# Optimization experiments

Measured on AMD Instinct MI355X. Metric: run time of the kernel, lower is better.

The kernel has to match this reference:

```python
import jax, jax.numpy as jnp
import numpy as np

B, T, D = 8, 16, 1024
N, K, H = 16, 8, 128   # q heads, kv heads, head dim
S = 8192               # cache size
CUR = 4096             # tokens already in cache
ROPE_THETA = 1000000
EPS = 1e-6
LARGE_NEGATIVE = jnp.finfo(jnp.bfloat16).min


def setup_inputs() -> dict:
    key = jax.random.key(0)
    ks = jax.random.split(key, 8)
    w = 0.02  # realistic weight scale
    return {
        "x": jax.random.normal(ks[0], (B, T, D), jnp.float32),
        "Wq": jax.random.normal(ks[1], (D, N, H), jnp.float32) * w,
        "Wk": jax.random.normal(ks[2], (D, K, H), jnp.float32) * w,
        "Wv": jax.random.normal(ks[3], (D, K, H), jnp.float32) * w,
        "Wo": jax.random.normal(ks[4], (N, H, D), jnp.float32) * w,
        "q_scale": jnp.ones((H,), jnp.float32),
        "k_scale": jnp.ones((H,), jnp.float32),
        "k_cache": jax.random.normal(ks[5], (B, S, K, H), jnp.float32),
        "v_cache": jax.random.normal(ks[6], (B, S, K, H), jnp.float32),
        "segment_ids": jnp.ones((B, T), jnp.int32),
        "start_ind": jnp.zeros((B,), jnp.int32),  # already resolved (= left_pads)
        "cur_ind": CUR,
    }


def _rmsnorm(x, scale, eps=EPS):
    xf = x.astype(jnp.float32)
    y = xf * jax.lax.rsqrt(jnp.mean(xf * xf, axis=-1, keepdims=True) + eps)
    return (y * scale).astype(x.dtype)


def _rope_sincos(positions, head_dim):
    frac = jnp.arange(0, head_dim, 2, dtype=jnp.float32) / head_dim
    inv_freq = 1.0 / (ROPE_THETA ** frac)
    ang = jnp.einsum("BT,k->BTk", positions.astype(jnp.float32), inv_freq,
                     precision=jax.lax.Precision.HIGHEST)
    return jnp.sin(ang), jnp.cos(ang)


def _apply_rope(x, sin, cos):
    x1, x2 = x[..., : x.shape[-1] // 2], x[..., x.shape[-1] // 2 :]
    sin, cos = sin[:, :, None, :], cos[:, :, None, :]
    return jnp.concatenate([x1 * cos - x2 * sin, x2 * cos + x1 * sin], axis=-1).astype(x.dtype)


def reference(x, Wq, Wk, Wv, Wo, q_scale, k_scale, k_cache, v_cache,
              segment_ids, start_ind, cur_ind):
    b, t, _ = x.shape
    n_rep = N // K
    scale = H ** -0.5

    # projections + per-head RMSNorm on q/k
    q = _rmsnorm(jnp.einsum("BTD,DNH->BTNH", x, Wq), q_scale)
    k = _rmsnorm(jnp.einsum("BSD,DKH->BSKH", x, Wk), k_scale)
    v = jnp.einsum("BSD,DKH->BSKH", x, Wv)

    # start index: resolved from left pads on first call
    left_pads = jnp.sum(jnp.cumsum(segment_ids != 0, axis=-1) == 0, -1).astype(jnp.int32)
    start = jnp.where(start_ind < 0, left_pads, start_ind)

    # positions from segment ids, offset by cache cursor
    rel = jax.vmap(lambda row: jnp.where(row != 0, jnp.arange(t) - jnp.argmax(row), 2 ** 30))(segment_ids)
    pos = rel + cur_ind
    sin, cos = _rope_sincos(pos, H)
    q = _apply_rope(q, sin, cos)
    k = _apply_rope(k, sin, cos)

    # KV cache append
    kc = jax.lax.dynamic_update_slice(k_cache, k, (0, cur_ind, 0, 0))
    vc = jax.lax.dynamic_update_slice(v_cache, v, (0, cur_ind, 0, 0))

    # GQA attention against full cache
    qg = q.reshape((b, t, K, n_rep, H))
    logits = jnp.einsum("BTKGH,BSKH->BTSKG", qg, kc) * scale

    q_pos = cur_ind + jnp.arange(t, dtype=jnp.int32)[None, :] - start[:, None]
    ts = jnp.arange(S, dtype=jnp.int32)
    kv_seg = (ts[None, :] >= start[:, None]) & (ts[None, :] < cur_ind + t)
    k_pos = ts[None, :] - start[:, None]
    causal = k_pos[:, None, :] <= q_pos[:, :, None]
    seg_mask = kv_seg[:, None, :] == segment_ids[:, :, None]
    mask = (causal & seg_mask)[:, :, :, None, None]

    logits = jnp.where(mask, logits, LARGE_NEGATIVE)
    w = jax.nn.softmax(logits.astype(jnp.float32), axis=2).astype(logits.dtype)
    o = jnp.einsum("BTSKG,BSKH->BTKGH", w, vc).reshape((b, t, N, H))
    return jnp.einsum("BTNH,NHD->BTD", o, Wo)
```

## Files before the change

kernel.cpp:

```cpp
#include <hip/hip_runtime.h>

#define BB 8
#define TT 16
#define DD 1024
#define NN 16
#define KHN 8
#define HH 128
#define SS 8192
#define NPART 8

typedef __attribute__((ext_vector_type(8))) short bf16x8;
typedef __attribute__((ext_vector_type(4))) float f32x4;

__device__ __forceinline__ unsigned short f2bf(float f) {
  unsigned u = __builtin_bit_cast(unsigned, f);
  u += 0x7FFFu + ((u >> 16) & 1u);
  return (unsigned short)(u >> 16);
}
__device__ __forceinline__ float bf2f(unsigned short h) {
  unsigned u = ((unsigned)h) << 16;
  return __builtin_bit_cast(float, u);
}
__device__ __forceinline__ f32x4 mfma16(bf16x8 a, bf16x8 b, f32x4 c) {
  return __builtin_amdgcn_mfma_f32_16x16x32_bf16(a, b, c, 0, 0, 0);
}
__device__ __forceinline__ void pack4(unsigned short* dst, float a, float b, float c, float d) {
  unsigned lo = (unsigned)f2bf(a) | ((unsigned)f2bf(b) << 16);
  unsigned hi = (unsigned)f2bf(c) | ((unsigned)f2bf(d) << 16);
  *(uint2*)dst = make_uint2(lo, hi);
}

__global__ __launch_bounds__(256) void k_qkv_gemm(
    const float* __restrict__ x, const float* __restrict__ Wq,
    const float* __restrict__ Wk, const float* __restrict__ Wv,
    float* __restrict__ qkv) {
  __shared__ __align__(16) unsigned short Al[32][40];
  __shared__ __align__(16) unsigned short Bl[32][132];
  const int tid = threadIdx.x;
  const int lane = tid & 63, wv = tid >> 6;
  const int cc = lane & 15, g = lane >> 4;
  const int m0 = blockIdx.x * 32;
  const int cbk = blockIdx.y;
  const float* Wsrc;
  int ldw, n0;
  if (cbk < 16)      { Wsrc = Wq; ldw = 2048; n0 = cbk * 128; }
  else if (cbk < 24) { Wsrc = Wk; ldw = 1024; n0 = (cbk - 16) * 128; }
  else               { Wsrc = Wv; ldw = 1024; n0 = (cbk - 24) * 128; }
  const int rt = wv >> 1, cb0 = (wv & 1) * 64;
  f32x4 acc[4];
#pragma unroll
  for (int i = 0; i < 4; ++i) acc[i] = (f32x4)0.0f;

  for (int k0 = 0; k0 < 1024; k0 += 32) {
    {
      int r = tid >> 3, c4 = (tid & 7) << 2;
      float4 f = *(const float4*)(x + (m0 + r) * 1024 + k0 + c4);
      pack4(&Al[r][c4], f.x, f.y, f.z, f.w);
    }
#pragma unroll
    for (int i = 0; i < 4; ++i) {
      int ch = tid + (i << 8);
      int r = ch >> 5, c4 = (ch & 31) << 2;
      float4 f = *(const float4*)(Wsrc + (size_t)(k0 + r) * ldw + n0 + c4);
      pack4(&Bl[r][c4], f.x, f.y, f.z, f.w);
    }
    __syncthreads();
    bf16x8 af = *(const bf16x8*)&Al[rt * 16 + cc][g * 8];
#pragma unroll
    for (int ct = 0; ct < 4; ++ct) {
      bf16x8 bf;
#pragma unroll
      for (int j = 0; j < 8; ++j) bf[j] = (short)Bl[g * 8 + j][cb0 + ct * 16 + cc];
      acc[ct] = mfma16(af, bf, acc[ct]);
    }
    __syncthreads();
  }
#pragma unroll
  for (int ct = 0; ct < 4; ++ct)
#pragma unroll
    for (int r = 0; r < 4; ++r) {
      int row = m0 + rt * 16 + g * 4 + r;
      int col = cbk * 128 + cb0 + ct * 16 + cc;
      qkv[row * 4096 + col] = acc[ct][r];
    }
}

__global__ __launch_bounds__(128) void k_normrope(
    const float* __restrict__ qkv, const float* __restrict__ qs,
    const float* __restrict__ ks, const int* __restrict__ seg,
    const int* __restrict__ cur_p,
    unsigned short* __restrict__ qa, unsigned short* __restrict__ ka,
    unsigned short* __restrict__ va) {
  __shared__ float lv[128];
  __shared__ float red[2];
  const int row = blockIdx.x, b = row >> 4, t = row & 15;
  const int hid = blockIdx.y;
  const int h = threadIdx.x;
  float val;
  if (hid < 16)      val = qkv[row * 4096 + hid * 128 + h];
  else if (hid < 24) val = qkv[row * 4096 + 2048 + (hid - 16) * 128 + h];
  else               val = qkv[row * 4096 + 3072 + (hid - 24) * 128 + h];

  if (hid >= 24) {
    int kh = hid - 24;
    va[((b * KHN + kh) * TT + t) * 128 + h] = f2bf(val);
    return;
  }
  float ss = val * val;
#pragma unroll
  for (int m = 1; m < 64; m <<= 1) ss += __shfl_xor(ss, m, 64);
  int wid = threadIdx.x >> 6, lane = threadIdx.x & 63;
  if (lane == 0) red[wid] = ss;
  __syncthreads();
  float mean = (red[0] + red[1]) * (1.0f / 128.0f);
  float scl = (hid < 16) ? qs[h] : ks[h];
  float nrm = val * (1.0f / sqrtf(mean + 1e-6f)) * scl;
  lv[h] = nrm;
  __syncthreads();
  float prt = lv[h ^ 64];
  const int cur = cur_p[0];
  int first = TT;
#pragma unroll
  for (int i = TT - 1; i >= 0; --i)
    if (seg[b * TT + i] != 0) first = i;
  float posf;
  if (seg[b * TT + t] != 0) posf = (float)(t - first + cur);
  else                      posf = (float)(1073741824 + cur);
  int j = h & 63;
  float inv = powf(1.0e6f, -((float)j) * (1.0f / 64.0f));
  float ang = posf * inv;
  float sn = sinf(ang), cs = cosf(ang);
  float outv = (h < 64) ? (nrm * cs - prt * sn) : (nrm * cs + prt * sn);
  if (hid < 16) {
    int kh = hid >> 1, gq = hid & 1;
    qa[((b * KHN + kh) * 32 + gq * 16 + t) * 128 + h] =
        f2bf(outv * 0.08838834764831845f);
  } else {
    int kh = hid - 16;
    ka[((b * KHN + kh) * TT + t) * 128 + h] = f2bf(outv);
  }
}

__global__ __launch_bounds__(256, 2) void k_attn(
    const float* __restrict__ kcache, const float* __restrict__ vcache,
    const unsigned short* __restrict__ qa, const unsigned short* __restrict__ ka,
    const unsigned short* __restrict__ va, const int* __restrict__ seg,
    const int* __restrict__ sind, const int* __restrict__ cur_p,
    float* __restrict__ partO, float* __restrict__ partML) {
  __shared__ __align__(16) unsigned short Kl[4][32][132];
  __shared__ __align__(16) unsigned short Pl[4][32][40];
  __shared__ float mls[2][32][2];
  const int tid = threadIdx.x, wv = tid >> 6, lane = tid & 63;
  const int cc = lane & 15, g = lane >> 4;
  const int pair = blockIdx.x, b = pair >> 3, kh = pair & 7;
  const int qi = blockIdx.y;
  const int cur = cur_p[0];
  const int len = cur + TT;
  int start_b = sind[b];
  if (start_b < 0) {
    int first = TT;
#pragma unroll
    for (int i = TT - 1; i >= 0; --i)
      if (seg[b * TT + i] != 0) first = i;
    start_b = first;
  }
  const int NTt = (len + 31) >> 5;
  const int L = (NTt + NPART - 1) / NPART;
  const int tlo = qi * L;
  const int thi = (tlo + L < NTt) ? (tlo + L) : NTt;

  bf16x8 qf[2][4];
  {
    const unsigned short* qb = qa + ((size_t)pair * 32) * 128;
#pragma unroll
    for (int rb = 0; rb < 2; ++rb)
#pragma unroll
      for (int kk = 0; kk < 4; ++kk)
        qf[rb][kk] = *(const bf16x8*)(qb + (rb * 16 + cc) * 128 + kk * 32 + g * 8);
  }
  const float* kcb = kcache + (size_t)b * (SS * 1024) + kh * 128;
  const float* vcb = vcache + (size_t)b * (SS * 1024) + kh * 128;
  const unsigned short* knb = ka + (size_t)(b * KHN + kh) * (TT * 128);
  const unsigned short* vnb = va + (size_t)(b * KHN + kh) * (TT * 128);

  f32x4 acc[2][8];
  float mreg[2][4], lreg[2][4];
#pragma unroll
  for (int rb = 0; rb < 2; ++rb) {
#pragma unroll
    for (int hb = 0; hb < 8; ++hb) acc[rb][hb] = (f32x4)0.0f;
#pragma unroll
    for (int r = 0; r < 4; ++r) { mreg[rb][r] = -1e30f; lreg[rb][r] = 0.0f; }
  }

  for (int tile = tlo + wv; tile < thi; tile += 4) {
    const int ts0 = tile << 5;
    if (ts0 + 32 <= cur) {
#pragma unroll
      for (int i = 0; i < 16; ++i) {
        int ch = lane + (i << 6);
        int r = ch >> 5, c4 = (ch & 31) << 2;
        float4 f = *(const float4*)(kcb + (size_t)(ts0 + r) * 1024 + c4);
        pack4(&Kl[wv][r][c4], f.x, f.y, f.z, f.w);
      }
    } else {
#pragma unroll
      for (int i = 0; i < 16; ++i) {
        int ch = lane + (i << 6);
        int r = ch >> 5, c4 = (ch & 31) << 2;
        int ts = ts0 + r;
        if (ts < cur) {
          float4 f = *(const float4*)(kcb + (size_t)ts * 1024 + c4);
          pack4(&Kl[wv][r][c4], f.x, f.y, f.z, f.w);
        } else {
          int tr = ts - cur; if (tr > TT - 1) tr = TT - 1;
          ushort4 u = *(const ushort4*)(knb + tr * 128 + c4);
          *(ushort4*)&Kl[wv][r][c4] = u;
        }
      }
    }
    __builtin_amdgcn_wave_barrier();
    bf16x8 vf[8];
    if (ts0 + 32 <= cur) {
#pragma unroll
      for (int hb = 0; hb < 8; ++hb) {
        int hc = hb * 16 + cc;
#pragma unroll
        for (int j = 0; j < 8; ++j) {
          int ts = ts0 + g * 8 + j;
          vf[hb][j] = (short)f2bf(vcb[(size_t)ts * 1024 + hc]);
        }
      }
    } else {
#pragma unroll
      for (int hb = 0; hb < 8; ++hb) {
        int hc = hb * 16 + cc;
#pragma unroll
        for (int j = 0; j < 8; ++j) {
          int ts = ts0 + g * 8 + j;
          float vvf;
          if (ts < cur) vvf = vcb[(size_t)ts * 1024 + hc];
          else { int tr = ts - cur; if (tr > TT - 1) tr = TT - 1; vvf = bf2f(vnb[tr * 128 + hc]); }
          vf[hb][j] = (short)f2bf(vvf);
        }
      }
    }
    f32x4 s[2][2];
#pragma unroll
    for (int rb = 0; rb < 2; ++rb)
#pragma unroll
      for (int cb = 0; cb < 2; ++cb) s[rb][cb] = (f32x4)0.0f;
#pragma unroll
    for (int kk = 0; kk < 4; ++kk) {
#pragma unroll
      for (int cb = 0; cb < 2; ++cb) {
        const unsigned short* kp = &Kl[wv][cb * 16 + cc][kk * 32 + g * 8];
        uint2 lo = *(const uint2*)kp;
        uint2 hi = *(const uint2*)(kp + 4);
        bf16x8 kf = __builtin_bit_cast(bf16x8, make_uint4(lo.x, lo.y, hi.x, hi.y));
        s[0][cb] = mfma16(qf[0][kk], kf, s[0][cb]);
        s[1][cb] = mfma16(qf[1][kk], kf, s[1][cb]);
      }
    }
    float al[2][4];
#pragma unroll
    for (int rb = 0; rb < 2; ++rb) {
#pragma unroll
      for (int r = 0; r < 4; ++r) {
        const int tq = g * 4 + r;
#pragma unroll
        for (int cb = 0; cb < 2; ++cb) {
          int ts = ts0 + cb * 16 + cc;
          bool ok = (ts >= start_b) && (ts <= cur + tq);
          if (!ok) s[rb][cb][r] = -1e30f;
        }
        float tm = fmaxf(s[rb][0][r], s[rb][1][r]);
#pragma unroll
        for (int m = 1; m < 16; m <<= 1) tm = fmaxf(tm, __shfl_xor(tm, m, 64));
        float mn = fmaxf(mreg[rb][r], tm);
        float a = __expf(mreg[rb][r] - mn);
        float p0 = (s[rb][0][r] < -1e29f) ? 0.0f : __expf(s[rb][0][r] - mn);
        float p1 = (s[rb][1][r] < -1e29f) ? 0.0f : __expf(s[rb][1][r] - mn);
        s[rb][0][r] = p0; s[rb][1][r] = p1;
        float rs = p0 + p1;
#pragma unroll
        for (int m = 1; m < 16; m <<= 1) rs += __shfl_xor(rs, m, 64);
        lreg[rb][r] = lreg[rb][r] * a + rs;
        mreg[rb][r] = mn;
        al[rb][r] = a;
      }
    }
#pragma unroll
    for (int rb = 0; rb < 2; ++rb)
#pragma unroll
      for (int cb = 0; cb < 2; ++cb)
#pragma unroll
        for (int r = 0; r < 4; ++r)
          Pl[wv][rb * 16 + g * 4 + r][cb * 16 + cc] = f2bf(s[rb][cb][r]);
    __builtin_amdgcn_wave_barrier();
    bf16x8 pf[2];
#pragma unroll
    for (int rb = 0; rb < 2; ++rb)
      pf[rb] = *(const bf16x8*)&Pl[wv][rb * 16 + cc][g * 8];
#pragma unroll
    for (int rb = 0; rb < 2; ++rb)
#pragma unroll
      for (int hb = 0; hb < 8; ++hb) {
        f32x4 t = acc[rb][hb];
#pragma unroll
        for (int r = 0; r < 4; ++r) t[r] *= al[rb][r];
        acc[rb][hb] = mfma16(pf[rb], vf[hb], t);
      }
  }

  float* Oscr = (float*)&Kl[0][0][0];
  auto dump = [&](int sid) {
#pragma unroll
    for (int rb = 0; rb < 2; ++rb)
#pragma unroll
      for (int hb = 0; hb < 8; ++hb)
#pragma unroll
        for (int r = 0; r < 4; ++r)
          Oscr[(sid * 32 + rb * 16 + g * 4 + r) * 128 + hb * 16 + cc] = acc[rb][hb][r];
    if (cc == 0) {
#pragma unroll
      for (int rb = 0; rb < 2; ++rb)
#pragma unroll
        for (int r = 0; r < 4; ++r) {
          mls[sid][rb * 16 + g * 4 + r][0] = mreg[rb][r];
          mls[sid][rb * 16 + g * 4 + r][1] = lreg[rb][r];
        }
    }
  };
  auto mergefrom = [&](int sid) {
    float a0s[2][4], a1s[2][4];
#pragma unroll
    for (int rb = 0; rb < 2; ++rb)
#pragma unroll
      for (int r = 0; r < 4; ++r) {
        int row = rb * 16 + g * 4 + r;
        float mp = mls[sid][row][0], lp = mls[sid][row][1];
        float M = fmaxf(mreg[rb][r], mp);
        float a0 = __expf(mreg[rb][r] - M), a1 = __expf(mp - M);
        lreg[rb][r] = lreg[rb][r] * a0 + lp * a1;
        mreg[rb][r] = M;
        a0s[rb][r] = a0; a1s[rb][r] = a1;
      }
#pragma unroll
    for (int rb = 0; rb < 2; ++rb)
#pragma unroll
      for (int hb = 0; hb < 8; ++hb)
#pragma unroll
        for (int r = 0; r < 4; ++r) {
          int row = rb * 16 + g * 4 + r;
          acc[rb][hb][r] = acc[rb][hb][r] * a0s[rb][r] +
                           Oscr[(sid * 32 + row) * 128 + hb * 16 + cc] * a1s[rb][r];
        }
  };
  __syncthreads();
  if (wv >= 2) dump(wv - 2);
  __syncthreads();
  if (wv < 2) mergefrom(wv);
  __syncthreads();
  if (wv == 1) dump(0);
  __syncthreads();
  if (wv == 0) {
    mergefrom(0);
    size_t pidx = (size_t)pair * NPART + qi;
#pragma unroll
    for (int rb = 0; rb < 2; ++rb)
#pragma unroll
      for (int hb = 0; hb < 8; ++hb)
#pragma unroll
        for (int r = 0; r < 4; ++r)
          partO[(pidx * 32 + rb * 16 + g * 4 + r) * 128 + hb * 16 + cc] = acc[rb][hb][r];
    if (cc == 0) {
#pragma unroll
      for (int rb = 0; rb < 2; ++rb)
#pragma unroll
        for (int r = 0; r < 4; ++r) {
          partML[pidx * 64 + (rb * 16 + g * 4 + r) * 2 + 0] = mreg[rb][r];
          partML[pidx * 64 + (rb * 16 + g * 4 + r) * 2 + 1] = lreg[rb][r];
        }
    }
  }
}

__global__ __launch_bounds__(256) void k_combine(
    const float* __restrict__ partO, const float* __restrict__ partML,
    unsigned short* __restrict__ obf) {
  __shared__ float sc[NPART][32];
  const int pair = blockIdx.x, b = pair >> 3, kh = pair & 7;
  const int tid = threadIdx.x;
  if (tid < 32) {
    float mm[NPART], ll[NPART];
    float M = -3.0e38f;
#pragma unroll
    for (int p = 0; p < NPART; ++p) {
      mm[p] = partML[((size_t)pair * NPART + p) * 64 + tid * 2 + 0];
      ll[p] = partML[((size_t)pair * NPART + p) * 64 + tid * 2 + 1];
      M = fmaxf(M, mm[p]);
    }
    float denom = 0.0f;
#pragma unroll
    for (int p = 0; p < NPART; ++p) denom += __expf(mm[p] - M) * ll[p];
    float inv = (denom > 0.0f) ? 1.0f / denom : 0.0f;
#pragma unroll
    for (int p = 0; p < NPART; ++p) sc[p][tid] = __expf(mm[p] - M) * inv;
  }
  __syncthreads();
#pragma unroll
  for (int i = 0; i < 16; ++i) {
    int idx = tid + (i << 8);
    int row = idx >> 7, hc = idx & 127;
    float o = 0.0f;
#pragma unroll
    for (int p = 0; p < NPART; ++p)
      o += partO[(((size_t)pair * NPART + p) * 32 + row) * 128 + hc] * sc[p][row];
    int gq = row >> 4, t = row & 15, n = kh * 2 + gq;
    obf[((b * TT + t) * NN + n) * 128 + hc] = f2bf(o);
  }
}

__global__ __launch_bounds__(256) void k_out_gemm(
    const unsigned short* __restrict__ obf, const float* __restrict__ Wo,
    float* __restrict__ out) {
  __shared__ __align__(16) unsigned short Al[32][40];
  __shared__ __align__(16) unsigned short Bl[32][68];
  const int tid = threadIdx.x, lane = tid & 63, wv = tid >> 6;
  const int cc = lane & 15, g = lane >> 4;
  const int m0 = blockIdx.x * 32, n0 = blockIdx.y * 64;
  const int rt = wv >> 1, cb0 = (wv & 1) * 32;
  f32x4 acc[2];
#pragma unroll
  for (int i = 0; i < 2; ++i) acc[i] = (f32x4)0.0f;

  for (int k0 = 0; k0 < 2048; k0 += 32) {
    {
      int r = tid >> 3, c4 = (tid & 7) << 2;
      ushort4 u = *(const ushort4*)(obf + (m0 + r) * 2048 + k0 + c4);
      *(ushort4*)&Al[r][c4] = u;
    }
#pragma unroll
    for (int i = 0; i < 2; ++i) {
      int ch = tid + (i << 8);
      int r = ch >> 4, c4 = (ch & 15) << 2;
      float4 f = *(const float4*)(Wo + (size_t)(k0 + r) * 1024 + n0 + c4);
      pack4(&Bl[r][c4], f.x, f.y, f.z, f.w);
    }
    __syncthreads();
    bf16x8 af = *(const bf16x8*)&Al[rt * 16 + cc][g * 8];
#pragma unroll
    for (int ct = 0; ct < 2; ++ct) {
      bf16x8 bf;
#pragma unroll
      for (int j = 0; j < 8; ++j) bf[j] = (short)Bl[g * 8 + j][cb0 + ct * 16 + cc];
      acc[ct] = mfma16(af, bf, acc[ct]);
    }
    __syncthreads();
  }
#pragma unroll
  for (int ct = 0; ct < 2; ++ct)
#pragma unroll
    for (int r = 0; r < 4; ++r)
      out[(m0 + rt * 16 + g * 4 + r) * 1024 + n0 + cb0 + ct * 16 + cc] = acc[ct][r];
}

extern "C" void kernel_launch(void* const* d_in, const int* in_sizes, int n_in,
                              void* d_out, int out_size, void* d_ws, size_t ws_size,
                              hipStream_t stream) {
  (void)in_sizes; (void)n_in; (void)out_size; (void)ws_size;
  const float* x   = (const float*)d_in[0];
  const float* Wq  = (const float*)d_in[1];
  const float* Wk  = (const float*)d_in[2];
  const float* Wv  = (const float*)d_in[3];
  const float* Wo  = (const float*)d_in[4];
  const float* qs  = (const float*)d_in[5];
  const float* ks  = (const float*)d_in[6];
  const float* kc  = (const float*)d_in[7];
  const float* vc  = (const float*)d_in[8];
  const int* seg   = (const int*)d_in[9];
  const int* sind  = (const int*)d_in[10];
  const int* curp  = (const int*)d_in[11];
  float* out = (float*)d_out;

  char* ws = (char*)d_ws;
  float*          qkv    = (float*)(ws + 0);
  unsigned short* qa     = (unsigned short*)(ws + 2097152);
  unsigned short* ka     = (unsigned short*)(ws + 2621440);
  unsigned short* va     = (unsigned short*)(ws + 2883584);
  float*          partO  = (float*)(ws + 3145728);
  float*          partML = (float*)(ws + 11534336);
  unsigned short* obf    = (unsigned short*)(ws + 11665408);

  k_qkv_gemm<<<dim3(4, 32), 256, 0, stream>>>(x, Wq, Wk, Wv, qkv);
  k_normrope<<<dim3(128, 32), 128, 0, stream>>>(qkv, qs, ks, seg, curp, qa, ka, va);
  k_attn<<<dim3(64, NPART), 256, 0, stream>>>(kc, vc, qa, ka, va, seg, sind, curp, partO, partML);
  k_combine<<<64, 256, 0, stream>>>(partO, partML, obf);
  k_out_gemm<<<dim3(4, 16), 256, 0, stream>>>(obf, Wo, out);
}
```

Measured before the change: 168.9 us.

## Pre-transpose weights to bf16 K-major and drop LDS staging in GEMMs

Adds a kernel that converts Wq/Wk/Wv/Wo to bf16 and transposes them into N-major, K-contiguous layouts in workspace. Both projection GEMMs then load MFMA operands straight from global memory as 16-byte vectors, with no shared-memory staging and no __syncthreads. The combine kernel is also split across four times as many blocks for more parallelism. The trade-off is an extra full weight read and write pass on every call, plus GEMM operand reuse that now relies on cache hits instead of LDS.

```diff
diff --git a/kernel.cpp b/kernel.cpp
--- a/kernel.cpp
+++ b/kernel.cpp
@@ -30,58 +30,79 @@
   *(uint2*)dst = make_uint2(lo, hi);
 }
 
+__global__ __launch_bounds__(256) void k_wtrans(
+    const float* __restrict__ Wq, const float* __restrict__ Wk,
+    const float* __restrict__ Wv, const float* __restrict__ Wo,
+    unsigned short* __restrict__ Wt1, unsigned short* __restrict__ Wt2) {
+  __shared__ __align__(16) unsigned short Tl[64][66];
+  const int tid = threadIdx.x;
+  const int z = blockIdx.z;
+  const float* src; int K, N; unsigned short* dst;
+  if (z == 0)      { src = Wq; K = 1024; N = 2048; dst = Wt1; }
+  else if (z == 1) { src = Wk; K = 1024; N = 1024; dst = Wt1 + (size_t)2048 * 1024; }
+  else if (z == 2) { src = Wv; K = 1024; N = 1024; dst = Wt1 + (size_t)3072 * 1024; }
+  else             { src = Wo; K = 2048; N = 1024; dst = Wt2; }
+  const int n0 = blockIdx.x * 64, k0 = blockIdx.y * 64;
+  if (n0 >= N || k0 >= K) return;
+  {
+    const int r = tid >> 4, c4 = (tid & 15) << 2;
+#pragma unroll
+    for (int p = 0; p < 4; ++p) {
+      const int k = p * 16 + r;
+      float4 f = *(const float4*)(src + (size_t)(k0 + k) * N + n0 + c4);
+      pack4(&Tl[k][c4], f.x, f.y, f.z, f.w);
+    }
+  }
+  __syncthreads();
+  {
+    const int c8 = tid & 7, nb = tid >> 3;
+#pragma unroll
+    for (int p = 0; p < 2; ++p) {
+      const int n = p * 32 + nb;
+      unsigned short tmp[8];
+#pragma unroll
+      for (int j = 0; j < 8; ++j) tmp[j] = Tl[c8 * 8 + j][n];
+      unsigned short* dp = dst + (size_t)(n0 + n) * K + k0 + c8 * 8;
+      *(uint4*)dp = *(const uint4*)&tmp[0];
+    }
+  }
+}
+
 __global__ __launch_bounds__(256) void k_qkv_gemm(
-    const float* __restrict__ x, const float* __restrict__ Wq,
-    const float* __restrict__ Wk, const float* __restrict__ Wv,
+    const float* __restrict__ x, const unsigned short* __restrict__ Wt1,
     float* __restrict__ qkv) {
-  __shared__ __align__(16) unsigned short Al[32][40];
-  __shared__ __align__(16) unsigned short Bl[32][132];
-  const int tid = threadIdx.x;
-  const int lane = tid & 63, wv = tid >> 6;
+  const int tid = threadIdx.x, lane = tid & 63, wv = tid >> 6;
   const int cc = lane & 15, g = lane >> 4;
-  const int m0 = blockIdx.x * 32;
-  const int cbk = blockIdx.y;
-  const float* Wsrc;
-  int ldw, n0;
-  if (cbk < 16)      { Wsrc = Wq; ldw = 2048; n0 = cbk * 128; }
-  else if (cbk < 24) { Wsrc = Wk; ldw = 1024; n0 = (cbk - 16) * 128; }
-  else               { Wsrc = Wv; ldw = 1024; n0 = (cbk - 24) * 128; }
+  const int m0 = blockIdx.x * 32, n0 = blockIdx.y * 128;
   const int rt = wv >> 1, cb0 = (wv & 1) * 64;
+  const int m = m0 + rt * 16 + cc;
   f32x4 acc[4];
 #pragma unroll
   for (int i = 0; i < 4; ++i) acc[i] = (f32x4)0.0f;
 
+#pragma unroll 4
   for (int k0 = 0; k0 < 1024; k0 += 32) {
-    {
-      int r = tid >> 3, c4 = (tid & 7) << 2;
-      float4 f = *(const float4*)(x + (m0 + r) * 1024 + k0 + c4);
-      pack4(&Al[r][c4], f.x, f.y, f.z, f.w);
-    }
-#pragma unroll
-    for (int i = 0; i < 4; ++i) {
-      int ch = tid + (i << 8);
-      int r = ch >> 5, c4 = (ch & 31) << 2;
-      float4 f = *(const float4*)(Wsrc + (size_t)(k0 + r) * ldw + n0 + c4);
-      pack4(&Bl[r][c4], f.x, f.y, f.z, f.w);
-    }
-    __syncthreads();
-    bf16x8 af = *(const bf16x8*)&Al[rt * 16 + cc][g * 8];
+    float4 fa = *(const float4*)(x + (size_t)m * 1024 + k0 + g * 8);
+    float4 fb = *(const float4*)(x + (size_t)m * 1024 + k0 + g * 8 + 4);
+    bf16x8 af;
+    af[0] = (short)f2bf(fa.x); af[1] = (short)f2bf(fa.y);
+    af[2] = (short)f2bf(fa.z); af[3] = (short)f2bf(fa.w);
+    af[4] = (short)f2bf(fb.x); af[5] = (short)f2bf(fb.y);
+    af[6] = (short)f2bf(fb.z); af[7] = (short)f2bf(fb.w);
 #pragma unroll
     for (int ct = 0; ct < 4; ++ct) {
-      bf16x8 bf;
-#pragma unroll
-      for (int j = 0; j < 8; ++j) bf[j] = (short)Bl[g * 8 + j][cb0 + ct * 16 + cc];
+      const int n = n0 + cb0 + ct * 16 + cc;
+      bf16x8 bf = *(const bf16x8*)(Wt1 + (size_t)n * 1024 + k0 + g * 8);
       acc[ct] = mfma16(af, bf, acc[ct]);
     }
-    __syncthreads();
   }
 #pragma unroll
   for (int ct = 0; ct < 4; ++ct)
 #pragma unroll
     for (int r = 0; r < 4; ++r) {
       int row = m0 + rt * 16 + g * 4 + r;
-      int col = cbk * 128 + cb0 + ct * 16 + cc;
-      qkv[row * 4096 + col] = acc[ct][r];
+      int col = n0 + cb0 + ct * 16 + cc;
+      qkv[(size_t)row * 4096 + col] = acc[ct][r];
     }
 }
 
@@ -391,6 +412,7 @@
     unsigned short* __restrict__ obf) {
   __shared__ float sc[NPART][32];
   const int pair = blockIdx.x, b = pair >> 3, kh = pair & 7;
+  const int isub = blockIdx.y;
   const int tid = threadIdx.x;
   if (tid < 32) {
     float mm[NPART], ll[NPART];
@@ -410,8 +432,8 @@
   }
   __syncthreads();
 #pragma unroll
-  for (int i = 0; i < 16; ++i) {
-    int idx = tid + (i << 8);
+  for (int i = 0; i < 4; ++i) {
+    int idx = tid + ((isub * 4 + i) << 8);
     int row = idx >> 7, hc = idx & 127;
     float o = 0.0f;
 #pragma unroll
@@ -423,47 +445,32 @@
 }
 
 __global__ __launch_bounds__(256) void k_out_gemm(
-    const unsigned short* __restrict__ obf, const float* __restrict__ Wo,
+    const unsigned short* __restrict__ obf, const unsigned short* __restrict__ Wt2,
     float* __restrict__ out) {
-  __shared__ __align__(16) unsigned short Al[32][40];
-  __shared__ __align__(16) unsigned short Bl[32][68];
   const int tid = threadIdx.x, lane = tid & 63, wv = tid >> 6;
   const int cc = lane & 15, g = lane >> 4;
   const int m0 = blockIdx.x * 32, n0 = blockIdx.y * 64;
   const int rt = wv >> 1, cb0 = (wv & 1) * 32;
+  const int m = m0 + rt * 16 + cc;
   f32x4 acc[2];
 #pragma unroll
   for (int i = 0; i < 2; ++i) acc[i] = (f32x4)0.0f;
 
+#pragma unroll 4
   for (int k0 = 0; k0 < 2048; k0 += 32) {
-    {
-      int r = tid >> 3, c4 = (tid & 7) << 2;
-      ushort4 u = *(const ushort4*)(obf + (m0 + r) * 2048 + k0 + c4);
-      *(ushort4*)&Al[r][c4] = u;
-    }
-#pragma unroll
-    for (int i = 0; i < 2; ++i) {
-      int ch = tid + (i << 8);
-      int r = ch >> 4, c4 = (ch & 15) << 2;
-      float4 f = *(const float4*)(Wo + (size_t)(k0 + r) * 1024 + n0 + c4);
-      pack4(&Bl[r][c4], f.x, f.y, f.z, f.w);
-    }
-    __syncthreads();
-    bf16x8 af = *(const bf16x8*)&Al[rt * 16 + cc][g * 8];
+    bf16x8 af = *(const bf16x8*)(obf + (size_t)m * 2048 + k0 + g * 8);
 #pragma unroll
     for (int ct = 0; ct < 2; ++ct) {
-      bf16x8 bf;
-#pragma unroll
-      for (int j = 0; j < 8; ++j) bf[j] = (short)Bl[g * 8 + j][cb0 + ct * 16 + cc];
+      const int d = n0 + cb0 + ct * 16 + cc;
+      bf16x8 bf = *(const bf16x8*)(Wt2 + (size_t)d * 2048 + k0 + g * 8);
       acc[ct] = mfma16(af, bf, acc[ct]);
     }
-    __syncthreads();
   }
 #pragma unroll
   for (int ct = 0; ct < 2; ++ct)
 #pragma unroll
     for (int r = 0; r < 4; ++r)
-      out[(m0 + rt * 16 + g * 4 + r) * 1024 + n0 + cb0 + ct * 16 + cc] = acc[ct][r];
+      out[(size_t)(m0 + rt * 16 + g * 4 + r) * 1024 + n0 + cb0 + ct * 16 + cc] = acc[ct][r];
 }
 
 extern "C" void kernel_launch(void* const* d_in, const int* in_sizes, int n_in,
@@ -492,10 +499,13 @@
   float*          partO  = (float*)(ws + 3145728);
   float*          partML = (float*)(ws + 11534336);
   unsigned short* obf    = (unsigned short*)(ws + 11665408);
-
-  k_qkv_gemm<<<dim3(4, 32), 256, 0, stream>>>(x, Wq, Wk, Wv, qkv);
+  unsigned short* Wt1    = (unsigned short*)(ws + 12189696);
+  unsigned short* Wt2    = (unsigned short*)(ws + 20578304);
+
+  k_wtrans<<<dim3(32, 32, 4), 256, 0, stream>>>(Wq, Wk, Wv, Wo, Wt1, Wt2);
+  k_qkv_gemm<<<dim3(4, 32), 256, 0, stream>>>(x, Wt1, qkv);
   k_normrope<<<dim3(128, 32), 128, 0, stream>>>(qkv, qs, ks, seg, curp, qa, ka, va);
   k_attn<<<dim3(64, NPART), 256, 0, stream>>>(kc, vc, qa, ka, va, seg, sind, curp, partO, partML);
-  k_combine<<<64, 256, 0, stream>>>(partO, partML, obf);
-  k_out_gemm<<<dim3(4, 16), 256, 0, stream>>>(obf, Wo, out);
-}
+  k_combine<<<dim3(64, 4), 256, 0, stream>>>(partO, partML, obf);
+  k_out_gemm<<<dim3(4, 16), 256, 0, stream>>>(obf, Wt2, out);
+}
```

Result: faster. 139.4 us (-17.5%).
